# Performance work log

Hardware: AMD Instinct MI355X
Metric: run time of the kernel (lower is better)

## Reference

```python
import jax, jax.numpy as jnp
import numpy as np

TOP_K = 2

def setup_inputs() -> dict:
    key = jax.random.key(0)
    k1, k2 = jax.random.split(key)
    x = jax.random.normal(k1, (4, 4096, 4096), dtype=jnp.float32)
    # nn.Linear(hidden, experts, bias=False) weight: [num_experts, hidden]
    gate_w = jax.random.normal(k2, (64, 4096), dtype=jnp.float32) * (1.0 / np.sqrt(4096.0))
    return {"x": x, "gate_w": gate_w}

def reference(x, gate_w):
    # logits: [b, s, e] = x @ gate_w.T
    logits = jnp.einsum('bsh,eh->bse', x, gate_w)
    top_k_logits, top_k_indices = jax.lax.top_k(logits, TOP_K)  # [b, s, k]
    # softmax over top-k logits in float32, cast back to logits dtype
    probs = jax.nn.softmax(top_k_logits.astype(jnp.float32), axis=-1).astype(logits.dtype)
    return (logits, top_k_indices, probs)
```

## Files before the change

### kernel.cpp

```cpp
#include <hip/hip_runtime.h>
#include <math.h>

#define H 4096
#define E 64
#define BMROWS 32
#define NT 256
#define KQ 1024
#define BK 32
#define NWIN (KQ / BK)

typedef short bf16x8 __attribute__((ext_vector_type(8)));
typedef float f32x4  __attribute__((ext_vector_type(4)));

__device__ __forceinline__ unsigned f2bf_rne_u(float f) {
    unsigned u = __float_as_uint(f);
    return (u + 0x7fffu + ((u >> 16) & 1u)) >> 16;
}

__global__ __launch_bounds__(256) void convert_w(const float* __restrict__ w,
                                                 unsigned short* __restrict__ wh,
                                                 unsigned short* __restrict__ wl) {
    const int i = (blockIdx.x * 256 + threadIdx.x) * 4;
    float4 v = *(const float4*)(w + i);
    float vv[4] = {v.x, v.y, v.z, v.w};
    unsigned hh[4], ll[4];
#pragma unroll
    for (int j = 0; j < 4; ++j) {
        hh[j] = f2bf_rne_u(vv[j]);
        float r = vv[j] - __uint_as_float(hh[j] << 16);
        ll[j] = __float_as_uint(r) >> 16;
    }
    ushort4 h, l;
    h.x = (unsigned short)hh[0]; h.y = (unsigned short)hh[1];
    h.z = (unsigned short)hh[2]; h.w = (unsigned short)hh[3];
    l.x = (unsigned short)ll[0]; l.y = (unsigned short)ll[1];
    l.z = (unsigned short)ll[2]; l.w = (unsigned short)ll[3];
    *(ushort4*)(wh + i) = h;
    *(ushort4*)(wl + i) = l;
}

__device__ __forceinline__ void cvt8(const float4 a, const float4 b,
                                     bf16x8& hi, bf16x8& lo) {
    float v[8] = {a.x, a.y, a.z, a.w, b.x, b.y, b.z, b.w};
#pragma unroll
    for (int i = 0; i < 8; ++i) {
        unsigned h = f2bf_rne_u(v[i]);
        float r = v[i] - __uint_as_float(h << 16);
        unsigned l = __float_as_uint(r) >> 16;
        hi[i] = (short)h;
        lo[i] = (short)l;
    }
}

__global__ __launch_bounds__(NT, 2) void router_kernel(
    const float* __restrict__ x,
    const unsigned short* __restrict__ wh,
    const unsigned short* __restrict__ wl,
    float* __restrict__ out, int M)
{
    __shared__ __align__(16) f32x4 merge[8][4][64];

    const int t    = threadIdx.x;
    const int lane = t & 63;
    const int wk   = t >> 6;
    const int m0   = blockIdx.x * BMROWS;
    const int col  = lane & 15;
    const int quad = lane >> 4;

    const int kbase = wk * KQ + quad * 8;

    const float* xp0 = x + (size_t)(m0 + col) * H + kbase;
    const float* xp1 = x + (size_t)(m0 + 16 + col) * H + kbase;
    const unsigned short* whp = wh + (size_t)col * H + kbase;
    const unsigned short* wlp = wl + (size_t)col * H + kbase;

    f32x4 acc[2][4];
#pragma unroll
    for (int mt = 0; mt < 2; ++mt)
#pragma unroll
        for (int nt = 0; nt < 4; ++nt)
            acc[mt][nt] = (f32x4){0.0f, 0.0f, 0.0f, 0.0f};

    float4 xr[2][2];
    uint4  wrh[4], wrl[4];

    auto loadwin = [&](int win) {
        const int k = win * BK;
        xr[0][0] = *(const float4*)(xp0 + k);
        xr[0][1] = *(const float4*)(xp0 + k + 4);
        xr[1][0] = *(const float4*)(xp1 + k);
        xr[1][1] = *(const float4*)(xp1 + k + 4);
#pragma unroll
        for (int nt = 0; nt < 4; ++nt) {
            wrh[nt] = *(const uint4*)(whp + (size_t)(nt * 16) * H + k);
            wrl[nt] = *(const uint4*)(wlp + (size_t)(nt * 16) * H + k);
        }
    };

    loadwin(0);
#pragma unroll 2
    for (int win = 0; win < NWIN; ++win) {
        bf16x8 ah[2], al[2];
        cvt8(xr[0][0], xr[0][1], ah[0], al[0]);
        cvt8(xr[1][0], xr[1][1], ah[1], al[1]);
        bf16x8 bh[4], bl[4];
#pragma unroll
        for (int nt = 0; nt < 4; ++nt) {
            bh[nt] = __builtin_bit_cast(bf16x8, wrh[nt]);
            bl[nt] = __builtin_bit_cast(bf16x8, wrl[nt]);
        }

        if (win + 1 < NWIN) loadwin(win + 1);

#pragma unroll
        for (int nt = 0; nt < 4; ++nt) {
#pragma unroll
            for (int mt = 0; mt < 2; ++mt) {
                acc[mt][nt] = __builtin_amdgcn_mfma_f32_16x16x32_bf16(
                    ah[mt], bh[nt], acc[mt][nt], 0, 0, 0);
                acc[mt][nt] = __builtin_amdgcn_mfma_f32_16x16x32_bf16(
                    ah[mt], bl[nt], acc[mt][nt], 0, 0, 0);
                acc[mt][nt] = __builtin_amdgcn_mfma_f32_16x16x32_bf16(
                    al[mt], bh[nt], acc[mt][nt], 0, 0, 0);
            }
        }
    }

#pragma unroll
    for (int mt = 0; mt < 2; ++mt)
#pragma unroll
        for (int nt = 0; nt < 4; ++nt)
            merge[mt * 4 + nt][wk][lane] = acc[mt][nt];
    __syncthreads();

    if (wk != 0) return;

#pragma unroll
    for (int mt = 0; mt < 2; ++mt)
#pragma unroll
        for (int nt = 0; nt < 4; ++nt) {
#pragma unroll
            for (int w = 1; w < 4; ++w) {
                f32x4 o = merge[mt * 4 + nt][w][lane];
                acc[mt][nt] += o;
            }
        }

    float* logits   = out;
    float* idx_out  = out + (size_t)M * E;
    float* prob_out = idx_out + (size_t)M * 2;

#pragma unroll
    for (int mt = 0; mt < 2; ++mt) {
        const int mrow = m0 + mt * 16 + quad * 4;
#pragma unroll
        for (int r = 0; r < 4; ++r) {
#pragma unroll
            for (int nt = 0; nt < 4; ++nt)
                logits[(size_t)(mrow + r) * E + nt * 16 + col] = acc[mt][nt][r];

            float v1 = acc[mt][0][r], v2 = -INFINITY;
            int   i1 = col,           i2 = 0x7fffffff;
#pragma unroll
            for (int nt = 1; nt < 4; ++nt) {
                const float v = acc[mt][nt][r];
                const int   e = nt * 16 + col;
                if (v > v1)      { v2 = v1; i2 = i1; v1 = v; i1 = e; }
                else if (v > v2) { v2 = v;  i2 = e; }
            }
#pragma unroll
            for (int mask = 1; mask < 16; mask <<= 1) {
                const float ov1 = __shfl_xor(v1, mask);
                const float ov2 = __shfl_xor(v2, mask);
                const int   oi1 = __shfl_xor(i1, mask);
                const int   oi2 = __shfl_xor(i2, mask);
                const bool afirst = (v1 > ov1) || (v1 == ov1 && i1 < oi1);
                float nv1, nv2; int ni1, ni2;
                if (afirst) {
                    nv1 = v1; ni1 = i1;
                    const bool s = (v2 > ov1) || (v2 == ov1 && i2 < oi1);
                    nv2 = s ? v2 : ov1; ni2 = s ? i2 : oi1;
                } else {
                    nv1 = ov1; ni1 = oi1;
                    const bool s = (ov2 > v1) || (ov2 == v1 && oi2 < i1);
                    nv2 = s ? ov2 : v1; ni2 = s ? oi2 : i1;
                }
                v1 = nv1; v2 = nv2; i1 = ni1; i2 = ni2;
            }
            if (col == 0) {
                const int m = mrow + r;
                const float e2 = __expf(v2 - v1);
                const float d  = 1.0f + e2;
                *(float2*)(idx_out  + (size_t)m * 2) = make_float2((float)i1, (float)i2);
                *(float2*)(prob_out + (size_t)m * 2) = make_float2(1.0f / d, e2 / d);
            }
        }
    }
}

extern "C" void kernel_launch(void* const* d_in, const int* in_sizes, int n_in,
                              void* d_out, int out_size, void* d_ws, size_t ws_size,
                              hipStream_t stream) {
    const float* x = (const float*)d_in[0];
    const float* w = (const float*)d_in[1];
    unsigned short* wh = (unsigned short*)d_ws;
    unsigned short* wl = wh + (size_t)E * H;
    const int M = in_sizes[0] / H;

    hipLaunchKernelGGL(convert_w, dim3((E * H) / 1024), dim3(256), 0, stream,
                       w, wh, wl);
    hipLaunchKernelGGL(router_kernel, dim3(M / BMROWS), dim3(NT), 0, stream,
                       x, wh, wl, (float*)d_out, M);
}
```

Before: 407.0 us.

## Stage x tiles through double-buffered LDS and split waves by row tile

Replaces the per-wave K-split, in which each wave streamed its own quarter of K straight from global memory, with a block-wide coalesced load of 32x128 x tiles into a double-buffered, padded LDS buffer. Waves now split work as two row tiles by two K halves, so only a two-way merge is needed at the end. The goal is more coalesced global reads of x and better latency hiding through the prefetch. The cost is a __syncthreads per window, an extra trip through LDS, and weight loads that are issued inline instead of being prefetched into registers.

```diff
diff --git a/kernel.cpp b/kernel.cpp
--- a/kernel.cpp
+++ b/kernel.cpp
@@ -3,11 +3,11 @@
 
 #define H 4096
 #define E 64
-#define BMROWS 32
+#define BR 32
+#define BK 128
+#define LSTR 132
 #define NT 256
-#define KQ 1024
-#define BK 32
-#define NWIN (KQ / BK)
+#define NWIN (H / BK)
 
 typedef short bf16x8 __attribute__((ext_vector_type(8)));
 typedef float f32x4  __attribute__((ext_vector_type(4)));
@@ -58,142 +58,139 @@
     const unsigned short* __restrict__ wl,
     float* __restrict__ out, int M)
 {
-    __shared__ __align__(16) f32x4 merge[8][4][64];
+    __shared__ __align__(16) float xs[2][BR][LSTR];
+    __shared__ __align__(16) f32x4 mrg[8][64];
 
     const int t    = threadIdx.x;
     const int lane = t & 63;
-    const int wk   = t >> 6;
-    const int m0   = blockIdx.x * BMROWS;
+    const int wv   = t >> 6;
+    const int mt   = wv & 1;
+    const int kh   = wv >> 1;
     const int col  = lane & 15;
     const int quad = lane >> 4;
-
-    const int kbase = wk * KQ + quad * 8;
-
-    const float* xp0 = x + (size_t)(m0 + col) * H + kbase;
-    const float* xp1 = x + (size_t)(m0 + 16 + col) * H + kbase;
-    const unsigned short* whp = wh + (size_t)col * H + kbase;
-    const unsigned short* wlp = wl + (size_t)col * H + kbase;
-
-    f32x4 acc[2][4];
-#pragma unroll
-    for (int mt = 0; mt < 2; ++mt)
+    const int m0   = blockIdx.x * BR;
+
+    const float* xbase[4];
+    float*       lbase[4];
+#pragma unroll
+    for (int p = 0; p < 4; ++p) {
+        const int f   = t + NT * p;
+        const int row = f >> 5, ch = f & 31;
+        xbase[p] = x + (size_t)(m0 + row) * H + (ch << 2);
+        lbase[p] = &xs[0][row][ch << 2];
+    }
+    const int LBUF = BR * LSTR;
+
+    float4 xr[4];
+    auto stage_load = [&](int win) {
+#pragma unroll
+        for (int p = 0; p < 4; ++p)
+            xr[p] = *(const float4*)(xbase[p] + (size_t)win * BK);
+    };
+    auto stage_write = [&](int b) {
+#pragma unroll
+        for (int p = 0; p < 4; ++p)
+            *(float4*)(lbase[p] + b * LBUF) = xr[p];
+    };
+
+    const unsigned short* whp = wh + (size_t)col * H + quad * 8;
+    const unsigned short* wlp = wl + (size_t)col * H + quad * 8;
+
+    f32x4 acc[4];
+#pragma unroll
+    for (int nt = 0; nt < 4; ++nt) acc[nt] = (f32x4){0.0f, 0.0f, 0.0f, 0.0f};
+
+    const float* arow = &xs[0][mt * 16 + col][quad * 8];
+
+    stage_load(0);
+    stage_write(0);
+    __syncthreads();
+
+    for (int win = 0; win < NWIN; ++win) {
+        const int buf = win & 1;
+        if (win + 1 < NWIN) stage_load(win + 1);
+
+#pragma unroll
+        for (int si = 0; si < 2; ++si) {
+            const int s = kh * 2 + si;
+            const float* ap = arow + buf * LBUF + s * 32;
+            const float4 a0 = *(const float4*)ap;
+            const float4 a1 = *(const float4*)(ap + 4);
+            bf16x8 ah, al;
+            cvt8(a0, a1, ah, al);
+            const size_t kg = (size_t)win * BK + s * 32;
+#pragma unroll
+            for (int nt = 0; nt < 4; ++nt) {
+                const uint4 bhv = *(const uint4*)(whp + (size_t)(nt * 16) * H + kg);
+                const uint4 blv = *(const uint4*)(wlp + (size_t)(nt * 16) * H + kg);
+                const bf16x8 bh = __builtin_bit_cast(bf16x8, bhv);
+                const bf16x8 bl = __builtin_bit_cast(bf16x8, blv);
+                acc[nt] = __builtin_amdgcn_mfma_f32_16x16x32_bf16(ah, bh, acc[nt], 0, 0, 0);
+                acc[nt] = __builtin_amdgcn_mfma_f32_16x16x32_bf16(ah, bl, acc[nt], 0, 0, 0);
+                acc[nt] = __builtin_amdgcn_mfma_f32_16x16x32_bf16(al, bh, acc[nt], 0, 0, 0);
+            }
+        }
+
+        if (win + 1 < NWIN) stage_write(1 - buf);
+        __syncthreads();
+    }
+
+    if (kh == 1) {
 #pragma unroll
         for (int nt = 0; nt < 4; ++nt)
-            acc[mt][nt] = (f32x4){0.0f, 0.0f, 0.0f, 0.0f};
-
-    float4 xr[2][2];
-    uint4  wrh[4], wrl[4];
-
-    auto loadwin = [&](int win) {
-        const int k = win * BK;
-        xr[0][0] = *(const float4*)(xp0 + k);
-        xr[0][1] = *(const float4*)(xp0 + k + 4);
-        xr[1][0] = *(const float4*)(xp1 + k);
-        xr[1][1] = *(const float4*)(xp1 + k + 4);
-#pragma unroll
-        for (int nt = 0; nt < 4; ++nt) {
-            wrh[nt] = *(const uint4*)(whp + (size_t)(nt * 16) * H + k);
-            wrl[nt] = *(const uint4*)(wlp + (size_t)(nt * 16) * H + k);
-        }
-    };
-
-    loadwin(0);
-#pragma unroll 2
-    for (int win = 0; win < NWIN; ++win) {
-        bf16x8 ah[2], al[2];
-        cvt8(xr[0][0], xr[0][1], ah[0], al[0]);
-        cvt8(xr[1][0], xr[1][1], ah[1], al[1]);
-        bf16x8 bh[4], bl[4];
-#pragma unroll
-        for (int nt = 0; nt < 4; ++nt) {
-            bh[nt] = __builtin_bit_cast(bf16x8, wrh[nt]);
-            bl[nt] = __builtin_bit_cast(bf16x8, wrl[nt]);
-        }
-
-        if (win + 1 < NWIN) loadwin(win + 1);
-
-#pragma unroll
-        for (int nt = 0; nt < 4; ++nt) {
-#pragma unroll
-            for (int mt = 0; mt < 2; ++mt) {
-                acc[mt][nt] = __builtin_amdgcn_mfma_f32_16x16x32_bf16(
-                    ah[mt], bh[nt], acc[mt][nt], 0, 0, 0);
-                acc[mt][nt] = __builtin_amdgcn_mfma_f32_16x16x32_bf16(
-                    ah[mt], bl[nt], acc[mt][nt], 0, 0, 0);
-                acc[mt][nt] = __builtin_amdgcn_mfma_f32_16x16x32_bf16(
-                    al[mt], bh[nt], acc[mt][nt], 0, 0, 0);
-            }
-        }
-    }
-
-#pragma unroll
-    for (int mt = 0; mt < 2; ++mt)
-#pragma unroll
-        for (int nt = 0; nt < 4; ++nt)
-            merge[mt * 4 + nt][wk][lane] = acc[mt][nt];
+            mrg[mt * 4 + nt][lane] = acc[nt];
+    }
     __syncthreads();
-
-    if (wk != 0) return;
-
-#pragma unroll
-    for (int mt = 0; mt < 2; ++mt)
-#pragma unroll
-        for (int nt = 0; nt < 4; ++nt) {
-#pragma unroll
-            for (int w = 1; w < 4; ++w) {
-                f32x4 o = merge[mt * 4 + nt][w][lane];
-                acc[mt][nt] += o;
-            }
-        }
+    if (kh == 1) return;
+#pragma unroll
+    for (int nt = 0; nt < 4; ++nt)
+        acc[nt] += mrg[mt * 4 + nt][lane];
 
     float* logits   = out;
     float* idx_out  = out + (size_t)M * E;
     float* prob_out = idx_out + (size_t)M * 2;
 
-#pragma unroll
-    for (int mt = 0; mt < 2; ++mt) {
-        const int mrow = m0 + mt * 16 + quad * 4;
-#pragma unroll
-        for (int r = 0; r < 4; ++r) {
-#pragma unroll
-            for (int nt = 0; nt < 4; ++nt)
-                logits[(size_t)(mrow + r) * E + nt * 16 + col] = acc[mt][nt][r];
-
-            float v1 = acc[mt][0][r], v2 = -INFINITY;
-            int   i1 = col,           i2 = 0x7fffffff;
-#pragma unroll
-            for (int nt = 1; nt < 4; ++nt) {
-                const float v = acc[mt][nt][r];
-                const int   e = nt * 16 + col;
-                if (v > v1)      { v2 = v1; i2 = i1; v1 = v; i1 = e; }
-                else if (v > v2) { v2 = v;  i2 = e; }
+    const int mrow0 = m0 + mt * 16 + quad * 4;
+#pragma unroll
+    for (int r = 0; r < 4; ++r) {
+        const int m = mrow0 + r;
+#pragma unroll
+        for (int nt = 0; nt < 4; ++nt)
+            logits[(size_t)m * E + nt * 16 + col] = acc[nt][r];
+
+        float v1 = acc[0][r], v2 = -INFINITY;
+        int   i1 = col,       i2 = 0x7fffffff;
+#pragma unroll
+        for (int nt = 1; nt < 4; ++nt) {
+            const float v = acc[nt][r];
+            const int   e = nt * 16 + col;
+            if (v > v1)      { v2 = v1; i2 = i1; v1 = v; i1 = e; }
+            else if (v > v2) { v2 = v;  i2 = e; }
+        }
+#pragma unroll
+        for (int mask = 1; mask < 16; mask <<= 1) {
+            const float ov1 = __shfl_xor(v1, mask);
+            const float ov2 = __shfl_xor(v2, mask);
+            const int   oi1 = __shfl_xor(i1, mask);
+            const int   oi2 = __shfl_xor(i2, mask);
+            const bool afirst = (v1 > ov1) || (v1 == ov1 && i1 < oi1);
+            float nv1, nv2; int ni1, ni2;
+            if (afirst) {
+                nv1 = v1; ni1 = i1;
+                const bool s = (v2 > ov1) || (v2 == ov1 && i2 < oi1);
+                nv2 = s ? v2 : ov1; ni2 = s ? i2 : oi1;
+            } else {
+                nv1 = ov1; ni1 = oi1;
+                const bool s = (ov2 > v1) || (ov2 == v1 && oi2 < i1);
+                nv2 = s ? ov2 : v1; ni2 = s ? oi2 : i1;
             }
-#pragma unroll
-            for (int mask = 1; mask < 16; mask <<= 1) {
-                const float ov1 = __shfl_xor(v1, mask);
-                const float ov2 = __shfl_xor(v2, mask);
-                const int   oi1 = __shfl_xor(i1, mask);
-                const int   oi2 = __shfl_xor(i2, mask);
-                const bool afirst = (v1 > ov1) || (v1 == ov1 && i1 < oi1);
-                float nv1, nv2; int ni1, ni2;
-                if (afirst) {
-                    nv1 = v1; ni1 = i1;
-                    const bool s = (v2 > ov1) || (v2 == ov1 && i2 < oi1);
-                    nv2 = s ? v2 : ov1; ni2 = s ? i2 : oi1;
-                } else {
-                    nv1 = ov1; ni1 = oi1;
-                    const bool s = (ov2 > v1) || (ov2 == v1 && oi2 < i1);
-                    nv2 = s ? ov2 : v1; ni2 = s ? oi2 : i1;
-                }
-                v1 = nv1; v2 = nv2; i1 = ni1; i2 = ni2;
-            }
-            if (col == 0) {
-                const int m = mrow + r;
-                const float e2 = __expf(v2 - v1);
-                const float d  = 1.0f + e2;
-                *(float2*)(idx_out  + (size_t)m * 2) = make_float2((float)i1, (float)i2);
-                *(float2*)(prob_out + (size_t)m * 2) = make_float2(1.0f / d, e2 / d);
-            }
+            v1 = nv1; v2 = nv2; i1 = ni1; i2 = ni2;
+        }
+        if (col == 0) {
+            const float e2 = __expf(v2 - v1);
+            const float d  = 1.0f + e2;
+            *(float2*)(idx_out  + (size_t)m * 2) = make_float2((float)i1, (float)i2);
+            *(float2*)(prob_out + (size_t)m * 2) = make_float2(1.0f / d, e2 / d);
         }
     }
 }
@@ -209,6 +206,6 @@
 
     hipLaunchKernelGGL(convert_w, dim3((E * H) / 1024), dim3(256), 0, stream,
                        w, wh, wl);
-    hipLaunchKernelGGL(router_kernel, dim3(M / BMROWS), dim3(NT), 0, stream,
+    hipLaunchKernelGGL(router_kernel, dim3(M / BR), dim3(NT), 0, stream,
                        x, wh, wl, (float*)d_out, M);
 }
```

After: 513.2 us. 26.1% more time.

## Halve rows per block and deepen x prefetch to four windows

Applied to the files above, without the earlier changes.

Each block now handles 16 rows instead of 32, doubling the grid and raising the occupancy hint to 4 blocks per SIMD. The x loads are prefetched four windows ahead through a ring of registers, while weight loads stay one window ahead, to hide more HBM latency. The cost is that each weight tile is reused for half as many rows, so weight traffic through L2 doubles.

```diff
diff --git a/kernel.cpp b/kernel.cpp
--- a/kernel.cpp
+++ b/kernel.cpp
@@ -3,11 +3,12 @@
 
 #define H 4096
 #define E 64
-#define BMROWS 32
+#define BR 16
 #define NT 256
-#define KQ 1024
+#define KQ (H / 4)
 #define BK 32
 #define NWIN (KQ / BK)
+#define PF 4
 
 typedef short bf16x8 __attribute__((ext_vector_type(8)));
 typedef float f32x4  __attribute__((ext_vector_type(4)));
@@ -52,148 +53,135 @@
     }
 }
 
-__global__ __launch_bounds__(NT, 2) void router_kernel(
+__global__ __launch_bounds__(NT, 4) void router_kernel(
     const float* __restrict__ x,
     const unsigned short* __restrict__ wh,
     const unsigned short* __restrict__ wl,
     float* __restrict__ out, int M)
 {
-    __shared__ __align__(16) f32x4 merge[8][4][64];
+    __shared__ __align__(16) f32x4 mrg[4][4][64];
 
     const int t    = threadIdx.x;
     const int lane = t & 63;
     const int wk   = t >> 6;
-    const int m0   = blockIdx.x * BMROWS;
     const int col  = lane & 15;
     const int quad = lane >> 4;
+    const int m0   = blockIdx.x * BR;
 
     const int kbase = wk * KQ + quad * 8;
-
-    const float* xp0 = x + (size_t)(m0 + col) * H + kbase;
-    const float* xp1 = x + (size_t)(m0 + 16 + col) * H + kbase;
+    const float*          xp  = x  + (size_t)(m0 + col) * H + kbase;
     const unsigned short* whp = wh + (size_t)col * H + kbase;
     const unsigned short* wlp = wl + (size_t)col * H + kbase;
 
-    f32x4 acc[2][4];
-#pragma unroll
-    for (int mt = 0; mt < 2; ++mt)
-#pragma unroll
-        for (int nt = 0; nt < 4; ++nt)
-            acc[mt][nt] = (f32x4){0.0f, 0.0f, 0.0f, 0.0f};
-
-    float4 xr[2][2];
-    uint4  wrh[4], wrl[4];
-
-    auto loadwin = [&](int win) {
-        const int k = win * BK;
-        xr[0][0] = *(const float4*)(xp0 + k);
-        xr[0][1] = *(const float4*)(xp0 + k + 4);
-        xr[1][0] = *(const float4*)(xp1 + k);
-        xr[1][1] = *(const float4*)(xp1 + k + 4);
+    f32x4 acc[4];
+#pragma unroll
+    for (int nt = 0; nt < 4; ++nt) acc[nt] = (f32x4){0.0f, 0.0f, 0.0f, 0.0f};
+
+    float4 xr[PF][2];
+    uint4  brh[4], brl[4];
+
+#pragma unroll
+    for (int p = 0; p < PF; ++p) {
+        xr[p][0] = *(const float4*)(xp + p * BK);
+        xr[p][1] = *(const float4*)(xp + p * BK + 4);
+    }
+#pragma unroll
+    for (int nt = 0; nt < 4; ++nt) {
+        brh[nt] = *(const uint4*)(whp + (size_t)(nt * 16) * H);
+        brl[nt] = *(const uint4*)(wlp + (size_t)(nt * 16) * H);
+    }
+
+#pragma unroll 4
+    for (int win = 0; win < NWIN; ++win) {
+        const int slot = win & (PF - 1);
+
+        bf16x8 ah, al;
+        cvt8(xr[slot][0], xr[slot][1], ah, al);
+        bf16x8 bh[4], bl[4];
 #pragma unroll
         for (int nt = 0; nt < 4; ++nt) {
-            wrh[nt] = *(const uint4*)(whp + (size_t)(nt * 16) * H + k);
-            wrl[nt] = *(const uint4*)(wlp + (size_t)(nt * 16) * H + k);
-        }
-    };
-
-    loadwin(0);
-#pragma unroll 2
-    for (int win = 0; win < NWIN; ++win) {
-        bf16x8 ah[2], al[2];
-        cvt8(xr[0][0], xr[0][1], ah[0], al[0]);
-        cvt8(xr[1][0], xr[1][1], ah[1], al[1]);
-        bf16x8 bh[4], bl[4];
+            bh[nt] = __builtin_bit_cast(bf16x8, brh[nt]);
+            bl[nt] = __builtin_bit_cast(bf16x8, brl[nt]);
+        }
+
+        if (win + PF < NWIN) {
+            xr[slot][0] = *(const float4*)(xp + (win + PF) * BK);
+            xr[slot][1] = *(const float4*)(xp + (win + PF) * BK + 4);
+        }
+        if (win + 1 < NWIN) {
+            const int k = (win + 1) * BK;
+#pragma unroll
+            for (int nt = 0; nt < 4; ++nt) {
+                brh[nt] = *(const uint4*)(whp + (size_t)(nt * 16) * H + k);
+                brl[nt] = *(const uint4*)(wlp + (size_t)(nt * 16) * H + k);
+            }
+        }
+
 #pragma unroll
         for (int nt = 0; nt < 4; ++nt) {
-            bh[nt] = __builtin_bit_cast(bf16x8, wrh[nt]);
-            bl[nt] = __builtin_bit_cast(bf16x8, wrl[nt]);
-        }
-
-        if (win + 1 < NWIN) loadwin(win + 1);
-
-#pragma unroll
-        for (int nt = 0; nt < 4; ++nt) {
-#pragma unroll
-            for (int mt = 0; mt < 2; ++mt) {
-                acc[mt][nt] = __builtin_amdgcn_mfma_f32_16x16x32_bf16(
-                    ah[mt], bh[nt], acc[mt][nt], 0, 0, 0);
-                acc[mt][nt] = __builtin_amdgcn_mfma_f32_16x16x32_bf16(
-                    ah[mt], bl[nt], acc[mt][nt], 0, 0, 0);
-                acc[mt][nt] = __builtin_amdgcn_mfma_f32_16x16x32_bf16(
-                    al[mt], bh[nt], acc[mt][nt], 0, 0, 0);
-            }
-        }
-    }
-
-#pragma unroll
-    for (int mt = 0; mt < 2; ++mt)
-#pragma unroll
-        for (int nt = 0; nt < 4; ++nt)
-            merge[mt * 4 + nt][wk][lane] = acc[mt][nt];
+            acc[nt] = __builtin_amdgcn_mfma_f32_16x16x32_bf16(ah, bh[nt], acc[nt], 0, 0, 0);
+            acc[nt] = __builtin_amdgcn_mfma_f32_16x16x32_bf16(ah, bl[nt], acc[nt], 0, 0, 0);
+            acc[nt] = __builtin_amdgcn_mfma_f32_16x16x32_bf16(al, bh[nt], acc[nt], 0, 0, 0);
+        }
+    }
+
+#pragma unroll
+    for (int nt = 0; nt < 4; ++nt)
+        mrg[nt][wk][lane] = acc[nt];
     __syncthreads();
-
     if (wk != 0) return;
 
 #pragma unroll
-    for (int mt = 0; mt < 2; ++mt)
-#pragma unroll
-        for (int nt = 0; nt < 4; ++nt) {
-#pragma unroll
-            for (int w = 1; w < 4; ++w) {
-                f32x4 o = merge[mt * 4 + nt][w][lane];
-                acc[mt][nt] += o;
-            }
-        }
+    for (int nt = 0; nt < 4; ++nt)
+#pragma unroll
+        for (int w = 1; w < 4; ++w)
+            acc[nt] += mrg[nt][w][lane];
 
     float* logits   = out;
     float* idx_out  = out + (size_t)M * E;
     float* prob_out = idx_out + (size_t)M * 2;
 
-#pragma unroll
-    for (int mt = 0; mt < 2; ++mt) {
-        const int mrow = m0 + mt * 16 + quad * 4;
-#pragma unroll
-        for (int r = 0; r < 4; ++r) {
-#pragma unroll
-            for (int nt = 0; nt < 4; ++nt)
-                logits[(size_t)(mrow + r) * E + nt * 16 + col] = acc[mt][nt][r];
-
-            float v1 = acc[mt][0][r], v2 = -INFINITY;
-            int   i1 = col,           i2 = 0x7fffffff;
-#pragma unroll
-            for (int nt = 1; nt < 4; ++nt) {
-                const float v = acc[mt][nt][r];
-                const int   e = nt * 16 + col;
-                if (v > v1)      { v2 = v1; i2 = i1; v1 = v; i1 = e; }
-                else if (v > v2) { v2 = v;  i2 = e; }
+    const int mrow0 = m0 + quad * 4;
+#pragma unroll
+    for (int r = 0; r < 4; ++r) {
+        const int m = mrow0 + r;
+#pragma unroll
+        for (int nt = 0; nt < 4; ++nt)
+            logits[(size_t)m * E + nt * 16 + col] = acc[nt][r];
+
+        float v1 = acc[0][r], v2 = -INFINITY;
+        int   i1 = col,       i2 = 0x7fffffff;
+#pragma unroll
+        for (int nt = 1; nt < 4; ++nt) {
+            const float v = acc[nt][r];
+            const int   e = nt * 16 + col;
+            if (v > v1)      { v2 = v1; i2 = i1; v1 = v; i1 = e; }
+            else if (v > v2) { v2 = v;  i2 = e; }
+        }
+#pragma unroll
+        for (int mask = 1; mask < 16; mask <<= 1) {
+            const float ov1 = __shfl_xor(v1, mask);
+            const float ov2 = __shfl_xor(v2, mask);
+            const int   oi1 = __shfl_xor(i1, mask);
+            const int   oi2 = __shfl_xor(i2, mask);
+            const bool afirst = (v1 > ov1) || (v1 == ov1 && i1 < oi1);
+            float nv1, nv2; int ni1, ni2;
+            if (afirst) {
+                nv1 = v1; ni1 = i1;
+                const bool s = (v2 > ov1) || (v2 == ov1 && i2 < oi1);
+                nv2 = s ? v2 : ov1; ni2 = s ? i2 : oi1;
+            } else {
+                nv1 = ov1; ni1 = oi1;
+                const bool s = (ov2 > v1) || (ov2 == v1 && oi2 < i1);
+                nv2 = s ? ov2 : v1; ni2 = s ? oi2 : i1;
             }
-#pragma unroll
-            for (int mask = 1; mask < 16; mask <<= 1) {
-                const float ov1 = __shfl_xor(v1, mask);
-                const float ov2 = __shfl_xor(v2, mask);
-                const int   oi1 = __shfl_xor(i1, mask);
-                const int   oi2 = __shfl_xor(i2, mask);
-                const bool afirst = (v1 > ov1) || (v1 == ov1 && i1 < oi1);
-                float nv1, nv2; int ni1, ni2;
-                if (afirst) {
-                    nv1 = v1; ni1 = i1;
-                    const bool s = (v2 > ov1) || (v2 == ov1 && i2 < oi1);
-                    nv2 = s ? v2 : ov1; ni2 = s ? i2 : oi1;
-                } else {
-                    nv1 = ov1; ni1 = oi1;
-                    const bool s = (ov2 > v1) || (ov2 == v1 && oi2 < i1);
-                    nv2 = s ? ov2 : v1; ni2 = s ? oi2 : i1;
-                }
-                v1 = nv1; v2 = nv2; i1 = ni1; i2 = ni2;
-            }
-            if (col == 0) {
-                const int m = mrow + r;
-                const float e2 = __expf(v2 - v1);
-                const float d  = 1.0f + e2;
-                *(float2*)(idx_out  + (size_t)m * 2) = make_float2((float)i1, (float)i2);
-                *(float2*)(prob_out + (size_t)m * 2) = make_float2(1.0f / d, e2 / d);
-            }
+            v1 = nv1; v2 = nv2; i1 = ni1; i2 = ni2;
+        }
+        if (col == 0) {
+            const float e2 = __expf(v2 - v1);
+            const float d  = 1.0f + e2;
+            *(float2*)(idx_out  + (size_t)m * 2) = make_float2((float)i1, (float)i2);
+            *(float2*)(prob_out + (size_t)m * 2) = make_float2(1.0f / d, e2 / d);
         }
     }
 }
@@ -209,6 +197,6 @@
 
     hipLaunchKernelGGL(convert_w, dim3((E * H) / 1024), dim3(256), 0, stream,
                        w, wh, wl);
-    hipLaunchKernelGGL(router_kernel, dim3(M / BMROWS), dim3(NT), 0, stream,
+    hipLaunchKernelGGL(router_kernel, dim3(M / BR), dim3(NT), 0, stream,
                        x, wh, wl, (float*)d_out, M);
 }
```

After: 495.6 us. 1.22x slower.
